# Performance work log

Hardware: AMD Instinct MI355X
Metric: run time of the kernel (lower is better)

Reference implementation:

```python
import jax, jax.numpy as jnp
import numpy as np

N_NODES = 50000
N_EDGES = 1600000
IN_CH = 128
OUT_SZ = 64


def setup_inputs() -> dict:
    key = jax.random.key(0)
    ks = jax.random.split(key, 10)
    seq = jax.random.normal(ks[0], (N_NODES, IN_CH), dtype=jnp.float32)
    edge_index = jax.random.randint(ks[1], (2, N_EDGES), 0, N_NODES, dtype=jnp.int64)
    s = 1.0 / np.sqrt(IN_CH)
    W_seq = jax.random.uniform(ks[2], (OUT_SZ, IN_CH), jnp.float32, -s, s)
    so = 1.0 / np.sqrt(OUT_SZ)
    w_f1 = jax.random.uniform(ks[3], (OUT_SZ,), jnp.float32, -so, so)
    b_f1 = jax.random.uniform(ks[4], (), jnp.float32, -so, so)
    w_f2 = jax.random.uniform(ks[5], (OUT_SZ,), jnp.float32, -so, so)
    b_f2 = jax.random.uniform(ks[6], (), jnp.float32, -so, so)
    bias = jnp.zeros((OUT_SZ,), jnp.float32)
    W_res = jax.random.uniform(ks[7], (OUT_SZ, IN_CH), jnp.float32, -s, s)
    b_res = jax.random.uniform(ks[8], (OUT_SZ,), jnp.float32, -s, s)
    return {"seq": seq, "edge_index": edge_index, "W_seq": W_seq,
            "w_f1": w_f1, "b_f1": b_f1, "w_f2": w_f2, "b_f2": b_f2,
            "bias": bias, "W_res": W_res, "b_res": b_res}


def reference(seq, edge_index, W_seq, w_f1, b_f1, w_f2, b_f2, bias, W_res, b_res):
    # seq: (N, in_ch); 1x1 conv == linear map per node
    seq_fts = jnp.einsum('ni,oi->no', seq, W_seq)          # (N, out)
    f1 = seq_fts @ w_f1 + b_f1                              # (N,)
    f2 = seq_fts @ w_f2 + b_f2                              # (N,)
    src, dst = edge_index[0], edge_index[1]
    e = jax.nn.leaky_relu(f1[src] + f2[dst], negative_slope=0.01)  # (E,)
    # NOTE: global softmax over all edges, as in the original (not per-node)
    coefs = jax.nn.softmax(e)                               # (E,)
    weighted = coefs[:, None] * seq_fts[dst]                # (E, out)
    vals = jax.ops.segment_sum(weighted, src, num_segments=seq.shape[0])  # (N, out)
    ret = vals + bias
    # residual: in_channel != out_sz -> 1x1 conv with bias
    ret = ret + jnp.einsum('ni,oi->no', seq, W_res) + b_res
    return jax.nn.elu(ret)
```

## Files before the change

kernel.cpp:

```cpp
#include <hip/hip_runtime.h>
#include <hip/hip_bf16.h>
#include <hip/hip_fp8.h>
#include <math.h>

#define N_NODES 50000
#define N_EDGES 1600000
#define IN_CH 128
#define OUT_SZ 64
#define N_TILES 3125

#define NBK 196
#define EPB 4096
#define NBL 391
#define CAP 10240

typedef short bf16x8 __attribute__((ext_vector_type(8)));
typedef float f32x4  __attribute__((ext_vector_type(4)));

__device__ __forceinline__ unsigned fenc(float x) {
    unsigned u = __float_as_uint(x);
    return (u & 0x80000000u) ? ~u : (u | 0x80000000u);
}
__device__ __forceinline__ float fdec(unsigned u) {
    return __uint_as_float((u & 0x80000000u) ? (u & 0x7fffffffu) : ~u);
}

__device__ __forceinline__ short bfbits(float x) {
    union { __hip_bfloat16 h; short s; } u;
    u.h = __float2bfloat16(x);
    return u.s;
}
__device__ __forceinline__ bf16x8 pack8(const float* f) {
    bf16x8 r;
#pragma unroll
    for (int j = 0; j < 8; ++j) r[j] = bfbits(f[j]);
    return r;
}

__global__ __launch_bounds__(256) void k_zero(unsigned* pmax1, unsigned* pmax2,
                                              float* psum, unsigned* bcur) {
    const int t = threadIdx.x;
    if (t < NBK) bcur[t * 16] = (unsigned)t * CAP;
    if (t == 0) { *pmax1 = 0u; *pmax2 = 0u; *psum = 0.0f; }
}

__global__ __launch_bounds__(256) void k_coarseA(const int* __restrict__ ei,
                                                 unsigned* __restrict__ bcur,
                                                 unsigned* __restrict__ pairs) {
    __shared__ unsigned buf[EPB];
    __shared__ unsigned hcnt[NBK];
    __shared__ unsigned hoff[NBK];
    const int t = threadIdx.x;
    const int blk = blockIdx.x;
    if (t < NBK) hcnt[t] = 0u;
    __syncthreads();
#pragma unroll
    for (int k = 0; k < 4; ++k) {
        int idx4 = k * 256 + t;
        int e4 = blk * EPB + idx4 * 4;
        if (e4 < N_EDGES) {
            int4 s = *(const int4*)(ei + e4);
            int4 d = *(const int4*)(ei + N_EDGES + e4);
            buf[idx4 * 4 + 0] = ((unsigned)s.x << 16) | (unsigned)d.x;
            buf[idx4 * 4 + 1] = ((unsigned)s.y << 16) | (unsigned)d.y;
            buf[idx4 * 4 + 2] = ((unsigned)s.z << 16) | (unsigned)d.z;
            buf[idx4 * 4 + 3] = ((unsigned)s.w << 16) | (unsigned)d.w;
            atomicAdd(&hcnt[s.x >> 8], 1u);
            atomicAdd(&hcnt[s.y >> 8], 1u);
            atomicAdd(&hcnt[s.z >> 8], 1u);
            atomicAdd(&hcnt[s.w >> 8], 1u);
        }
    }
    __syncthreads();
    if (t < NBK) {
        unsigned c = hcnt[t];
        hoff[t] = c ? atomicAdd(&bcur[t * 16], c) : 0u;
        hcnt[t] = 0u;
    }
    __syncthreads();
#pragma unroll
    for (int k = 0; k < 4; ++k) {
        int idx4 = k * 256 + t;
        int e4 = blk * EPB + idx4 * 4;
        if (e4 < N_EDGES) {
#pragma unroll
            for (int j = 0; j < 4; ++j) {
                unsigned p = buf[idx4 * 4 + j];
                unsigned b = p >> 24;
                unsigned lp = atomicAdd(&hcnt[b], 1u);
                pairs[hoff[b] + lp] = p;
            }
        }
    }
}

__global__ __launch_bounds__(256) void k_gemm(
    const float* __restrict__ seq, const float* __restrict__ Wseq,
    const float* __restrict__ Wres, const float* __restrict__ wf1,
    const float* __restrict__ bf1, const float* __restrict__ wf2,
    const float* __restrict__ bf2, const float* __restrict__ bias,
    const float* __restrict__ bres,
    __hip_fp8_e4m3* __restrict__ sfp8, float* __restrict__ f1,
    float* __restrict__ f2, unsigned* pmax1, unsigned* pmax2,
    float* __restrict__ out)
{
    __shared__ bf16x8 WL[2048];
    __shared__ float smax[8];
    const int t = threadIdx.x;

#pragma unroll
    for (int j = 0; j < 8; ++j) {
        int idx = t + j * 256;
        int ct = idx >> 8;
        int ks = (idx >> 6) & 3;
        int li = idx & 63;
        int c = ct * 16 + (li & 15);
        int k0 = ks * 32 + (li >> 4) * 8;
        const float* src = (c < 64) ? (Wseq + c * IN_CH + k0)
                                    : (Wres + (c - 64) * IN_CH + k0);
        float tmp[8];
        *(float4*)tmp = *(const float4*)src;
        *(float4*)(tmp + 4) = *(const float4*)(src + 4);
        WL[idx] = pack8(tmp);
    }
    __syncthreads();

    const int l = t & 63;
    const int wv = t >> 6;
    const int tile = blockIdx.x * 4 + wv;
    const bool active = tile < N_TILES;
    float mx1 = -3.0e38f, mx2 = -3.0e38f;

    if (active) {
        const int row = tile * 16 + (l & 15);
        const int kbase = (l >> 4) * 8;
        f32x4 acc[8];
#pragma unroll
        for (int ct = 0; ct < 8; ++ct) acc[ct] = (f32x4){0.f, 0.f, 0.f, 0.f};

#pragma unroll
        for (int ks = 0; ks < 4; ++ks) {
            const float* ap = seq + (size_t)row * IN_CH + ks * 32 + kbase;
            float tmp[8];
            *(float4*)tmp = *(const float4*)ap;
            *(float4*)(tmp + 4) = *(const float4*)(ap + 4);
            bf16x8 af = pack8(tmp);
#pragma unroll
            for (int ct = 0; ct < 8; ++ct)
                acc[ct] = __builtin_amdgcn_mfma_f32_16x16x32_bf16(
                    af, WL[(ct * 4 + ks) * 64 + l], acc[ct], 0, 0, 0);
        }

        const int n0 = tile * 16;
        float w1v[4], w2v[4], bb[4];
#pragma unroll
        for (int ct = 0; ct < 4; ++ct) {
            int oc = ct * 16 + (l & 15);
            w1v[ct] = wf1[oc];
            w2v[ct] = wf2[oc];
            bb[ct] = bias[oc] + bres[oc];
        }
        const float B1 = bf1[0], B2 = bf2[0];
#pragma unroll
        for (int r = 0; r < 4; ++r) {
            int node = n0 + (l >> 4) * 4 + r;
            size_t o = (size_t)node * 64 + (l & 15);
#pragma unroll
            for (int ct = 0; ct < 4; ++ct) {
                sfp8[o + ct * 16] = __hip_fp8_e4m3(acc[ct][r]);
                out[o + ct * 16] = acc[ct + 4][r] + bb[ct];
            }
            float t1 = acc[0][r] * w1v[0] + acc[1][r] * w1v[1]
                     + acc[2][r] * w1v[2] + acc[3][r] * w1v[3];
            float t2 = acc[0][r] * w2v[0] + acc[1][r] * w2v[1]
                     + acc[2][r] * w2v[2] + acc[3][r] * w2v[3];
#pragma unroll
            for (int m = 8; m; m >>= 1) {
                t1 += __shfl_xor(t1, m);
                t2 += __shfl_xor(t2, m);
            }
            if ((l & 15) == 0) {
                float F1 = t1 + B1, F2 = t2 + B2;
                f1[node] = F1;
                f2[node] = F2;
                mx1 = fmaxf(mx1, F1);
                mx2 = fmaxf(mx2, F2);
            }
        }
    }

    mx1 = fmaxf(mx1, __shfl_xor(mx1, 16)); mx1 = fmaxf(mx1, __shfl_xor(mx1, 32));
    mx2 = fmaxf(mx2, __shfl_xor(mx2, 16)); mx2 = fmaxf(mx2, __shfl_xor(mx2, 32));
    if (l == 0) { smax[wv] = mx1; smax[4 + wv] = mx2; }
    __syncthreads();
    if (t == 0) {
        atomicMax(pmax1, fenc(fmaxf(fmaxf(smax[0], smax[1]), fmaxf(smax[2], smax[3]))));
        atomicMax(pmax2, fenc(fmaxf(fmaxf(smax[4], smax[5]), fmaxf(smax[6], smax[7]))));
    }
}

__global__ __launch_bounds__(256) void k_sortsum(
    const unsigned* __restrict__ pairs, const unsigned* __restrict__ bcur,
    const float* __restrict__ f1, const float* __restrict__ f2,
    const unsigned* __restrict__ pmax1, const unsigned* __restrict__ pmax2,
    unsigned* __restrict__ offs, unsigned* __restrict__ offsE,
    unsigned* __restrict__ sPair, float* psum)
{
    __shared__ unsigned cur[256];
    __shared__ unsigned bs[256];
    __shared__ float f1loc[256];
    __shared__ float red[4];
    const int t = threadIdx.x;
    const int b = blockIdx.x;
    const int nbase = b << 8;
    const unsigned eb = (unsigned)b * CAP;
    const unsigned ee = bcur[b * 16];

    cur[t] = 0u;
    {
        int n = nbase + t;
        f1loc[t] = (n < N_NODES) ? f1[n] : 0.f;
    }
    __syncthreads();

    for (unsigned i = eb + t; i < ee; i += 256)
        atomicAdd(&cur[(pairs[i] >> 16) & 255u], 1u);
    __syncthreads();

    unsigned v = cur[t];
    bs[t] = v;
    __syncthreads();
    for (int off = 1; off < 256; off <<= 1) {
        unsigned w = (t >= off) ? bs[t - off] : 0u;
        __syncthreads();
        bs[t] += w;
        __syncthreads();
    }
    unsigned o = eb + (bs[t] - v);
    {
        int n = nbase + t;
        if (n < N_NODES) { offs[n] = o; offsE[n] = o + v; }
    }
    __syncthreads();
    cur[t] = o;
    __syncthreads();

    float M = fdec(*pmax1) + fdec(*pmax2);
    M = (M > 0.f) ? M : 0.01f * M;
    float ls = 0.f;
    for (unsigned i = eb + t; i < ee; i += 256) {
        unsigned p = pairs[i];
        unsigned li = (p >> 16) & 255u;
        unsigned dst = p & 0xffffu;
        float x = f1loc[li] + f2[dst];
        x = (x > 0.f) ? x : 0.01f * x;
        float ex = __expf(x - M);
        ls += ex;
        unsigned pos = atomicAdd(&cur[li], 1u);
        sPair[pos] = ((unsigned)(unsigned short)bfbits(ex) << 16) | dst;
    }
#pragma unroll
    for (int off = 32; off; off >>= 1) ls += __shfl_xor(ls, off);
    if ((t & 63) == 0) red[t >> 6] = ls;
    __syncthreads();
    if (t == 0) {
        ls = red[0] + red[1] + red[2] + red[3];
        unsafeAtomicAdd(psum, ls);
    }
}

__global__ __launch_bounds__(256) void k_acc(
    const unsigned* __restrict__ offs, const unsigned* __restrict__ offsE,
    const unsigned* __restrict__ sPair, const __hip_fp8_e4m3* __restrict__ sfp8,
    const float* __restrict__ psum, float* __restrict__ out)
{
    const int lane = threadIdx.x & 63;
    const int n = (blockIdx.x * 256 + threadIdx.x) >> 6;
    if (n >= N_NODES) return;
    const float inv = 1.0f / (*psum);
    const unsigned b = offs[n];
    const unsigned e = offsE[n];

    float acc = 0.f;
    for (unsigned e0 = b; e0 < e; e0 += 64) {
        const int cnt = (int)min(64u, e - e0);
        unsigned p = 0u;
        if (lane < cnt) p = sPair[e0 + lane];
        const int nb = (cnt + 7) & ~7;
        for (int j = 0; j < nb; j += 8) {
            unsigned q0 = __shfl(p, j);
            unsigned q1 = __shfl(p, j + 1);
            unsigned q2 = __shfl(p, j + 2);
            unsigned q3 = __shfl(p, j + 3);
            unsigned q4 = __shfl(p, j + 4);
            unsigned q5 = __shfl(p, j + 5);
            unsigned q6 = __shfl(p, j + 6);
            unsigned q7 = __shfl(p, j + 7);
            float v0 = (float)sfp8[(size_t)(q0 & 0xffffu) * 64 + lane];
            float v1 = (float)sfp8[(size_t)(q1 & 0xffffu) * 64 + lane];
            float v2 = (float)sfp8[(size_t)(q2 & 0xffffu) * 64 + lane];
            float v3 = (float)sfp8[(size_t)(q3 & 0xffffu) * 64 + lane];
            float v4 = (float)sfp8[(size_t)(q4 & 0xffffu) * 64 + lane];
            float v5 = (float)sfp8[(size_t)(q5 & 0xffffu) * 64 + lane];
            float v6 = (float)sfp8[(size_t)(q6 & 0xffffu) * 64 + lane];
            float v7 = (float)sfp8[(size_t)(q7 & 0xffffu) * 64 + lane];
            acc = fmaf(__uint_as_float(q0 & 0xffff0000u), v0, acc);
            acc = fmaf(__uint_as_float(q1 & 0xffff0000u), v1, acc);
            acc = fmaf(__uint_as_float(q2 & 0xffff0000u), v2, acc);
            acc = fmaf(__uint_as_float(q3 & 0xffff0000u), v3, acc);
            acc = fmaf(__uint_as_float(q4 & 0xffff0000u), v4, acc);
            acc = fmaf(__uint_as_float(q5 & 0xffff0000u), v5, acc);
            acc = fmaf(__uint_as_float(q6 & 0xffff0000u), v6, acc);
            acc = fmaf(__uint_as_float(q7 & 0xffff0000u), v7, acc);
        }
    }
    const size_t idx = (size_t)n * 64 + lane;
    float x = out[idx] + acc * inv;
    out[idx] = (x > 0.f) ? x : expm1f(x);
}

extern "C" void kernel_launch(void* const* d_in, const int* in_sizes, int n_in,
                              void* d_out, int out_size, void* d_ws, size_t ws_size,
                              hipStream_t stream) {
    const float* seq  = (const float*)d_in[0];
    const int*   ei   = (const int*)d_in[1];
    const float* Wseq = (const float*)d_in[2];
    const float* wf1  = (const float*)d_in[3];
    const float* bf1  = (const float*)d_in[4];
    const float* wf2  = (const float*)d_in[5];
    const float* bf2  = (const float*)d_in[6];
    const float* bias = (const float*)d_in[7];
    const float* Wres = (const float*)d_in[8];
    const float* bres = (const float*)d_in[9];
    float* out = (float*)d_out;

    unsigned* pmax1     = (unsigned*)d_ws;
    unsigned* pmax2     = (unsigned*)d_ws + 1;
    float*    psum      = (float*)d_ws + 2;
    unsigned* bcur      = (unsigned*)d_ws + 16;
    unsigned* offs      = bcur + NBK * 16;
    unsigned* offsE     = offs + N_NODES;
    unsigned* pairs     = offsE + N_NODES;
    unsigned* sPair     = pairs + (size_t)NBK * CAP;
    __hip_fp8_e4m3* sfp8 = (__hip_fp8_e4m3*)(sPair + (size_t)NBK * CAP);
    float*    f1        = (float*)(sfp8 + (size_t)N_NODES * 64);
    float*    f2        = f1 + N_NODES;

    k_zero<<<1, 256, 0, stream>>>(pmax1, pmax2, psum, bcur);
    k_coarseA<<<NBL, 256, 0, stream>>>(ei, bcur, pairs);
    k_gemm<<<782, 256, 0, stream>>>(seq, Wseq, Wres, wf1, bf1, wf2, bf2, bias,
                                    bres, sfp8, f1, f2, pmax1, pmax2, out);
    k_sortsum<<<NBK, 256, 0, stream>>>(pairs, bcur, f1, f2, pmax1, pmax2,
                                       offs, offsE, sPair, psum);
    k_acc<<<12500, 256, 0, stream>>>(offs, offsE, sPair, sfp8, psum, out);
}
```

Measured before the change: 115.2 us.

## Shrink source buckets to 64 nodes to run more sort-sum blocks

```diff
diff --git a/kernel.cpp b/kernel.cpp
--- a/kernel.cpp
+++ b/kernel.cpp
@@ -9,10 +9,10 @@
 #define OUT_SZ 64
 #define N_TILES 3125
 
-#define NBK 196
+#define NBK 782
 #define EPB 4096
 #define NBL 391
-#define CAP 10240
+#define CAP 2560
 
 typedef short bf16x8 __attribute__((ext_vector_type(8)));
 typedef float f32x4  __attribute__((ext_vector_type(4)));
@@ -39,9 +39,9 @@
 
 __global__ __launch_bounds__(256) void k_zero(unsigned* pmax1, unsigned* pmax2,
                                               float* psum, unsigned* bcur) {
-    const int t = threadIdx.x;
-    if (t < NBK) bcur[t * 16] = (unsigned)t * CAP;
-    if (t == 0) { *pmax1 = 0u; *pmax2 = 0u; *psum = 0.0f; }
+    const int i = blockIdx.x * 256 + threadIdx.x;
+    if (i < NBK) bcur[i * 16] = (unsigned)i * CAP;
+    if (i == 0) { *pmax1 = 0u; *pmax2 = 0u; *psum = 0.0f; }
 }
 
 __global__ __launch_bounds__(256) void k_coarseA(const int* __restrict__ ei,
@@ -52,7 +52,7 @@
     __shared__ unsigned hoff[NBK];
     const int t = threadIdx.x;
     const int blk = blockIdx.x;
-    if (t < NBK) hcnt[t] = 0u;
+    for (int b = t; b < NBK; b += 256) hcnt[b] = 0u;
     __syncthreads();
 #pragma unroll
     for (int k = 0; k < 4; ++k) {
@@ -65,17 +65,17 @@
             buf[idx4 * 4 + 1] = ((unsigned)s.y << 16) | (unsigned)d.y;
             buf[idx4 * 4 + 2] = ((unsigned)s.z << 16) | (unsigned)d.z;
             buf[idx4 * 4 + 3] = ((unsigned)s.w << 16) | (unsigned)d.w;
-            atomicAdd(&hcnt[s.x >> 8], 1u);
-            atomicAdd(&hcnt[s.y >> 8], 1u);
-            atomicAdd(&hcnt[s.z >> 8], 1u);
-            atomicAdd(&hcnt[s.w >> 8], 1u);
-        }
-    }
-    __syncthreads();
-    if (t < NBK) {
-        unsigned c = hcnt[t];
-        hoff[t] = c ? atomicAdd(&bcur[t * 16], c) : 0u;
-        hcnt[t] = 0u;
+            atomicAdd(&hcnt[s.x >> 6], 1u);
+            atomicAdd(&hcnt[s.y >> 6], 1u);
+            atomicAdd(&hcnt[s.z >> 6], 1u);
+            atomicAdd(&hcnt[s.w >> 6], 1u);
+        }
+    }
+    __syncthreads();
+    for (int b = t; b < NBK; b += 256) {
+        unsigned c = hcnt[b];
+        hoff[b] = c ? atomicAdd(&bcur[b * 16], c) : 0u;
+        hcnt[b] = 0u;
     }
     __syncthreads();
 #pragma unroll
@@ -86,7 +86,7 @@
 #pragma unroll
             for (int j = 0; j < 4; ++j) {
                 unsigned p = buf[idx4 * 4 + j];
-                unsigned b = p >> 24;
+                unsigned b = p >> 22;
                 unsigned lp = atomicAdd(&hcnt[b], 1u);
                 pairs[hoff[b] + lp] = p;
             }
@@ -206,43 +206,39 @@
     unsigned* __restrict__ offs, unsigned* __restrict__ offsE,
     unsigned* __restrict__ sPair, float* psum)
 {
-    __shared__ unsigned cur[256];
-    __shared__ unsigned bs[256];
-    __shared__ float f1loc[256];
+    __shared__ unsigned cur[64];
+    __shared__ float f1loc[64];
     __shared__ float red[4];
     const int t = threadIdx.x;
     const int b = blockIdx.x;
-    const int nbase = b << 8;
+    const int nbase = b << 6;
     const unsigned eb = (unsigned)b * CAP;
     const unsigned ee = bcur[b * 16];
 
-    cur[t] = 0u;
-    {
+    if (t < 64) {
+        cur[t] = 0u;
         int n = nbase + t;
         f1loc[t] = (n < N_NODES) ? f1[n] : 0.f;
     }
     __syncthreads();
 
     for (unsigned i = eb + t; i < ee; i += 256)
-        atomicAdd(&cur[(pairs[i] >> 16) & 255u], 1u);
-    __syncthreads();
-
-    unsigned v = cur[t];
-    bs[t] = v;
-    __syncthreads();
-    for (int off = 1; off < 256; off <<= 1) {
-        unsigned w = (t >= off) ? bs[t - off] : 0u;
-        __syncthreads();
-        bs[t] += w;
-        __syncthreads();
-    }
-    unsigned o = eb + (bs[t] - v);
-    {
+        atomicAdd(&cur[(pairs[i] >> 16) & 63u], 1u);
+    __syncthreads();
+
+    if (t < 64) {
+        unsigned v = cur[t];
+        unsigned incl = v;
+#pragma unroll
+        for (int off = 1; off < 64; off <<= 1) {
+            unsigned w = __shfl_up(incl, off);
+            if (t >= off) incl += w;
+        }
+        unsigned o = eb + (incl - v);
         int n = nbase + t;
         if (n < N_NODES) { offs[n] = o; offsE[n] = o + v; }
-    }
-    __syncthreads();
-    cur[t] = o;
+        cur[t] = o;
+    }
     __syncthreads();
 
     float M = fdec(*pmax1) + fdec(*pmax2);
@@ -250,7 +246,7 @@
     float ls = 0.f;
     for (unsigned i = eb + t; i < ee; i += 256) {
         unsigned p = pairs[i];
-        unsigned li = (p >> 16) & 255u;
+        unsigned li = (p >> 16) & 63u;
         unsigned dst = p & 0xffffu;
         float x = f1loc[li] + f2[dst];
         x = (x > 0.f) ? x : 0.01f * x;
@@ -346,7 +342,7 @@
     float*    f1        = (float*)(sfp8 + (size_t)N_NODES * 64);
     float*    f2        = f1 + N_NODES;
 
-    k_zero<<<1, 256, 0, stream>>>(pmax1, pmax2, psum, bcur);
+    k_zero<<<4, 256, 0, stream>>>(pmax1, pmax2, psum, bcur);
     k_coarseA<<<NBL, 256, 0, stream>>>(ei, bcur, pairs);
     k_gemm<<<782, 256, 0, stream>>>(seq, Wseq, Wres, wf1, bf1, wf2, bf2, bias,
                                     bres, sfp8, f1, f2, pmax1, pmax2, out);
```

Result: slower. 125.4 us (+8.9%).
